# Performance work log

Hardware: AMD Instinct MI355X
Metric: run time of the kernel (lower is better)

Reference implementation:

```python
import jax, jax.numpy as jnp
import numpy as np

N = 100000   # nodes per ntype
E = 1600000  # edges per etype (avg degree 16)
D = 128      # in_channels == hid_channels
LN_EPS = 1e-5


def setup_inputs() -> dict:
    key = jax.random.key(0)
    k = jax.random.split(key, 16)
    scale = 1.0 / np.sqrt(D)
    inp = {
        "x_A": jax.random.normal(k[0], (N, D), jnp.float32),
        "x_B": jax.random.normal(k[1], (N, D), jnp.float32),
        # per-etype GraphConv weights, etype order: [aa, ab, ba, bb]
        "W0": jax.random.normal(k[2], (4, D, D), jnp.float32) * scale,
        "b0": jnp.zeros((4, D), jnp.float32),
        "W1": jax.random.normal(k[3], (4, D, D), jnp.float32) * scale,
        "b1": jnp.zeros((4, D), jnp.float32),
        # LayerNorm params: [layer, ntype(A=0,B=1), D]
        "ln_gamma": jnp.ones((2, 2, D), jnp.float32),
        "ln_beta": jnp.zeros((2, 2, D), jnp.float32),
        "src_aa": jax.random.randint(k[4], (E,), 0, N, jnp.int32),
        "dst_aa": jax.random.randint(k[5], (E,), 0, N, jnp.int32),
        "src_ab": jax.random.randint(k[6], (E,), 0, N, jnp.int32),
        "dst_ab": jax.random.randint(k[7], (E,), 0, N, jnp.int32),
        "src_ba": jax.random.randint(k[8], (E,), 0, N, jnp.int32),
        "dst_ba": jax.random.randint(k[9], (E,), 0, N, jnp.int32),
        "src_bb": jax.random.randint(k[10], (E,), 0, N, jnp.int32),
        "dst_bb": jax.random.randint(k[11], (E,), 0, N, jnp.int32),
    }
    return inp


def _layer_norm(x, g, b):
    m = jnp.mean(x, axis=-1, keepdims=True)
    v = jnp.var(x, axis=-1, keepdims=True)
    return (x - m) * jax.lax.rsqrt(v + LN_EPS) * g + b


def _graph_conv(x, W, b, src, dst, n_dst, act):
    # dgl GraphConv norm='both': D_dst^{-1/2} A D_src^{-1/2} X W + b
    deg_out = jnp.clip(jax.ops.segment_sum(jnp.ones_like(src, x.dtype), src, num_segments=x.shape[0]), 1.0)
    deg_in = jnp.clip(jax.ops.segment_sum(jnp.ones_like(dst, x.dtype), dst, num_segments=n_dst), 1.0)
    h = (x * jax.lax.rsqrt(deg_out)[:, None]) @ W            # transform first (in==out)
    agg = jax.ops.segment_sum(h[src], dst, num_segments=n_dst)
    out = agg * jax.lax.rsqrt(deg_in)[:, None] + b
    return jax.nn.relu(out) if act else out


def reference(x_A, x_B, W0, b0, W1, b1, ln_gamma, ln_beta,
              src_aa, dst_aa, src_ab, dst_ab, src_ba, dst_ba, src_bb, dst_bb):
    hA, hB = x_A, x_B
    for l, (W, bias) in enumerate([(W0, b0), (W1, b1)]):
        act = (l == 0)  # relu inside each GraphConv for all but the last layer
        # HeteroGraphConv aggregate='sum': sum per-relation (activated) outputs per dst ntype
        nA = _graph_conv(hA, W[0], bias[0], src_aa, dst_aa, N, act) + \
             _graph_conv(hB, W[2], bias[2], src_ba, dst_ba, N, act)
        nB = _graph_conv(hA, W[1], bias[1], src_ab, dst_ab, N, act) + \
             _graph_conv(hB, W[3], bias[3], src_bb, dst_bb, N, act)
        hA = _layer_norm(nA, ln_gamma[l, 0], ln_beta[l, 0])
        hB = _layer_norm(nB, ln_gamma[l, 1], ln_beta[l, 1])
        # dropout p=0.0 (eval) -> identity
    return jnp.stack([hA, hB])  # [ntype, N, D]
```

## Files before the change

kernel.cpp:

```cpp
#include <hip/hip_runtime.h>
#include <hip/hip_bf16.h>

#define D 128
typedef unsigned int uint;
typedef unsigned short ushort;
typedef unsigned char uchar;
typedef short short8 __attribute__((ext_vector_type(8)));
typedef float f32x4 __attribute__((ext_vector_type(4)));

#define BKT_SHIFT 8
#define NBMAX 512
#define PART_EPT 16
#define SCAT_CAP 8192

__device__ __forceinline__ ushort f2bf(float f) {
    uint u = __float_as_uint(f);
    return (ushort)((u + 0x7fffu + ((u >> 16) & 1u)) >> 16);
}
__device__ __forceinline__ float bf2f(uint s) { return __uint_as_float(s << 16); }

__global__ __launch_bounds__(256) void bhist4_k(
    const int* __restrict__ s0, const int* __restrict__ d0,
    const int* __restrict__ s1, const int* __restrict__ d1,
    const int* __restrict__ s2, const int* __restrict__ d2,
    const int* __restrict__ s3, const int* __restrict__ d3,
    int* __restrict__ bcs, int* __restrict__ bcd, int N, int E) {
    const int e = blockIdx.y;
    const int* sp = e == 0 ? s0 : e == 1 ? s1 : e == 2 ? s2 : s3;
    const int* dp = e == 0 ? d0 : e == 1 ? d1 : e == 2 ? d2 : d3;
    const int NB = (N + 255) >> BKT_SHIFT;
    __shared__ int hs[NBMAX], hd[NBMAX];
    for (int j = threadIdx.x; j < NBMAX; j += 256) { hs[j] = 0; hd[j] = 0; }
    __syncthreads();
    const int base = blockIdx.x * 8192;
#pragma unroll
    for (int k = 0; k < 8; ++k) {
        int idx = base + (k * 256 + threadIdx.x) * 4;
        if (idx + 4 <= E) {
            int4 s = *(const int4*)(sp + idx);
            int4 d = *(const int4*)(dp + idx);
            atomicAdd(&hs[s.x >> BKT_SHIFT], 1); atomicAdd(&hs[s.y >> BKT_SHIFT], 1);
            atomicAdd(&hs[s.z >> BKT_SHIFT], 1); atomicAdd(&hs[s.w >> BKT_SHIFT], 1);
            atomicAdd(&hd[d.x >> BKT_SHIFT], 1); atomicAdd(&hd[d.y >> BKT_SHIFT], 1);
            atomicAdd(&hd[d.z >> BKT_SHIFT], 1); atomicAdd(&hd[d.w >> BKT_SHIFT], 1);
        } else {
            for (int i = idx; i < E && i < idx + 4; ++i) {
                atomicAdd(&hs[sp[i] >> BKT_SHIFT], 1);
                atomicAdd(&hd[dp[i] >> BKT_SHIFT], 1);
            }
        }
    }
    __syncthreads();
    for (int j = threadIdx.x; j < NB; j += 256) {
        if (hs[j]) atomicAdd(&bcs[e * NBMAX + j], hs[j]);
        if (hd[j]) atomicAdd(&bcd[e * NBMAX + j], hd[j]);
    }
}

__global__ __launch_bounds__(512) void bscan_k(
    const int* __restrict__ bcs, const int* __restrict__ bcd,
    int* __restrict__ sbase, int* __restrict__ scur,
    int* __restrict__ dbase, int* __restrict__ dcur, int N) {
    const int e = blockIdx.y;
    const int side = blockIdx.x;
    const int NB = (N + 255) >> BKT_SHIFT;
    const int* in = (side ? bcd : bcs) + e * NBMAX;
    int* b0 = (side ? dbase : sbase) + e * NBMAX;
    int* c0 = (side ? dcur : scur) + e * NBMAX;
    const int tid = threadIdx.x, lane = tid & 63, wid = tid >> 6;
    int v = (tid < NB) ? in[tid] : 0;
    int x = v;
#pragma unroll
    for (int off = 1; off < 64; off <<= 1) {
        int t = __shfl_up(x, off);
        if (lane >= off) x += t;
    }
    __shared__ int ws[8];
    if (lane == 63) ws[wid] = x;
    __syncthreads();
    if (tid == 0) {
        int run = 0;
#pragma unroll
        for (int w = 0; w < 8; ++w) { int t = ws[w]; ws[w] = run; run += t; }
    }
    __syncthreads();
    int excl = ws[wid] + x - v;
    if (tid < NB) { b0[tid] = excl; c0[tid] = excl; }
}

__global__ __launch_bounds__(256) void part4_k(
    const int* __restrict__ s0, const int* __restrict__ d0,
    const int* __restrict__ s1, const int* __restrict__ d1,
    const int* __restrict__ s2, const int* __restrict__ d2,
    const int* __restrict__ s3, const int* __restrict__ d3,
    int* __restrict__ scur, int* __restrict__ dcur,
    uint* __restrict__ pd, uchar* __restrict__ ps, int N, int E) {
    const int e = blockIdx.y;
    const int* sp = e == 0 ? s0 : e == 1 ? s1 : e == 2 ? s2 : s3;
    const int* dp = e == 0 ? d0 : e == 1 ? d1 : e == 2 ? d2 : d3;
    const int NB = (N + 255) >> BKT_SHIFT;
    uint* ptd = pd + (size_t)e * E;
    uchar* pts = ps + (size_t)e * E;
    __shared__ int hd[NBMAX], hs[NBMAX];
    for (int j = threadIdx.x; j < NBMAX; j += 256) { hd[j] = 0; hs[j] = 0; }
    __syncthreads();
    int myd[PART_EPT], mys[PART_EPT], rkd[PART_EPT], rks[PART_EPT];
    const int base = blockIdx.x * (256 * PART_EPT);
#pragma unroll
    for (int k = 0; k < PART_EPT; ++k) {
        int idx = base + k * 256 + threadIdx.x;
        if (idx < E) {
            int d = dp[idx], s = sp[idx];
            myd[k] = d; mys[k] = s;
            rkd[k] = atomicAdd(&hd[d >> BKT_SHIFT], 1);
            rks[k] = atomicAdd(&hs[s >> BKT_SHIFT], 1);
        } else {
            myd[k] = -1;
        }
    }
    __syncthreads();
    for (int j = threadIdx.x; j < NB; j += 256) {
        int c = hd[j];
        if (c) hd[j] = atomicAdd(&dcur[e * NBMAX + j], c);
        c = hs[j];
        if (c) hs[j] = atomicAdd(&scur[e * NBMAX + j], c);
    }
    __syncthreads();
#pragma unroll
    for (int k = 0; k < PART_EPT; ++k) {
        if (myd[k] >= 0) {
            int d = myd[k], s = mys[k];
            ptd[(size_t)((uint)hd[d >> BKT_SHIFT] + (uint)rkd[k])] =
                ((uint)(d & 255) << 24) | (uint)s;
            pts[(size_t)((uint)hs[s >> BKT_SHIFT] + (uint)rks[k])] = (uchar)(s & 255);
        }
    }
}

__global__ __launch_bounds__(256) void scat4_k(
    const uint* __restrict__ pd, const int* __restrict__ dbase,
    const int* __restrict__ bcd, int* __restrict__ start_g,
    int* __restrict__ cnt_g, float* __restrict__ rs_in,
    int* __restrict__ csr, int N, int E) {
    const int e = blockIdx.y;
    const int b = blockIdx.x;
    const int node0 = b << BKT_SHIFT;
    const int nodes = min(256, N - node0);
    const uint* pt = pd + (size_t)e * E;
    int* out = csr + (size_t)e * E;
    const int csr_base = dbase[e * NBMAX + b];
    const int span = bcd[e * NBMAX + b];
    __shared__ int cnt[256];
    __shared__ int cur[256];
    __shared__ int woff[4];
    __shared__ int lcsr[SCAT_CAP];
    const int tid = threadIdx.x, lane = tid & 63, wid = tid >> 6;
    cnt[tid] = 0;
    __syncthreads();
    for (int i = tid; i < span; i += 256) atomicAdd(&cnt[pt[csr_base + i] >> 24], 1);
    __syncthreads();
    int c = cnt[tid];
    int x = c;
#pragma unroll
    for (int off = 1; off < 64; off <<= 1) {
        int t = __shfl_up(x, off);
        if (lane >= off) x += t;
    }
    if (lane == 63) woff[wid] = x;
    __syncthreads();
    if (tid == 0) {
        int run = 0;
#pragma unroll
        for (int w = 0; w < 4; ++w) { int t = woff[w]; woff[w] = run; run += t; }
    }
    __syncthreads();
    int loc = woff[wid] + x - c;
    cur[tid] = loc;
    if (tid < nodes) {
        int n = node0 + tid;
        start_g[(size_t)e * N + n] = csr_base + loc;
        cnt_g[(size_t)e * N + n] = c;
        rs_in[(size_t)e * N + n] = rsqrtf((float)max(c, 1));
    }
    __syncthreads();
    for (int i = tid; i < span; i += 256) {
        uint pk = pt[csr_base + i];
        int pos = atomicAdd(&cur[pk >> 24], 1);
        int s = (int)(pk & 0xFFFFFFu);
        if (pos < SCAT_CAP) lcsr[pos] = s;
        else out[csr_base + pos] = s;
    }
    __syncthreads();
    const int lim = span < SCAT_CAP ? span : SCAT_CAP;
    for (int i = tid; i < lim; i += 256) out[csr_base + i] = lcsr[i];
}

__global__ __launch_bounds__(256) void shist_k(
    const uchar* __restrict__ ps, const int* __restrict__ sbase,
    const int* __restrict__ bcs, float* __restrict__ rs_out, int N, int E) {
    const int e = blockIdx.y;
    const int b = blockIdx.x;
    const int node0 = b << BKT_SHIFT;
    const int nodes = min(256, N - node0);
    const uchar* pt = ps + (size_t)e * E;
    const int base = sbase[e * NBMAX + b];
    const int span = bcs[e * NBMAX + b];
    __shared__ int c[256];
    c[threadIdx.x] = 0;
    __syncthreads();
    for (int i = threadIdx.x; i < span; i += 256) atomicAdd(&c[pt[base + i]], 1);
    __syncthreads();
    if (threadIdx.x < nodes)
        rs_out[(size_t)e * N + node0 + threadIdx.x] = rsqrtf((float)max(c[threadIdx.x], 1));
}

__global__ __launch_bounds__(256) void wswz_k(const float* __restrict__ W0,
                                              const float* __restrict__ W1,
                                              ushort* __restrict__ WF) {
    int t = blockIdx.x * 256 + threadIdx.x;
    int lane = t & 63, kf = (t >> 6) & 3, ct = (t >> 8) & 7, e = (t >> 11) & 3, l = (t >> 13) & 1;
    const float* Ws = (l ? W1 : W0) + (size_t)e * D * D;
    int m = lane & 15, q = lane >> 4;
    const float* src = Ws + (size_t)(kf * 32 + q * 8) * D + ct * 16 + m;
    ushort v[8];
#pragma unroll
    for (int j = 0; j < 8; ++j) v[j] = f2bf(src[(size_t)j * D]);
    uint4 pk;
    pk.x = (uint)v[0] | ((uint)v[1] << 16);
    pk.y = (uint)v[2] | ((uint)v[3] << 16);
    pk.z = (uint)v[4] | ((uint)v[5] << 16);
    pk.w = (uint)v[6] | ((uint)v[7] << 16);
    *(uint4*)(WF + ((size_t)(l * 4 + e) * 2048 + (ct * 4 + kf) * 64 + lane) * 8) = pk;
}

__global__ __launch_bounds__(256) void gemm_pair_k(
    const float* __restrict__ XA, const float* __restrict__ XB,
    const ushort* __restrict__ WF,
    const float* __restrict__ rs,
    ushort* __restrict__ yb,
    int n) {
    const int p = blockIdx.y;
    const float* X = p ? XB : XA;
    const int e0 = 2 * p, e1 = 2 * p + 1;
    const short8* F0 = (const short8*)(WF + (size_t)e0 * 16384);
    const short8* F1 = (const short8*)(WF + (size_t)e1 * 16384);
    const float* rs0 = rs + (size_t)e0 * n;
    const float* rs1 = rs + (size_t)e1 * n;
    ushort* Y0 = yb + (size_t)e0 * n * D;
    ushort* Y1 = yb + (size_t)e1 * n * D;
    const int lane = threadIdx.x & 63;
    const int m = lane & 15, q = lane >> 4;
    const int wave = blockIdx.x * 4 + (threadIdx.x >> 6);
    const int nw = gridDim.x * 4;
    const int nstrips = (n + 15) >> 4;
    for (int sidx = wave; sidx < nstrips; sidx += nw) {
        const int r = sidx * 16 + m;
        const int rc = r < n ? r : n - 1;
        const float* xp = X + (size_t)rc * D + q * 8;
        short8 xf[4];
#pragma unroll
        for (int kf = 0; kf < 4; ++kf) {
            float4 u0 = *(const float4*)(xp + kf * 32);
            float4 u1 = *(const float4*)(xp + kf * 32 + 4);
            short8 v;
            v[0] = (short)f2bf(u0.x); v[1] = (short)f2bf(u0.y);
            v[2] = (short)f2bf(u0.z); v[3] = (short)f2bf(u0.w);
            v[4] = (short)f2bf(u1.x); v[5] = (short)f2bf(u1.y);
            v[6] = (short)f2bf(u1.z); v[7] = (short)f2bf(u1.w);
            xf[kf] = v;
        }
        f32x4 a0[8], a1[8];
#pragma unroll
        for (int ct = 0; ct < 8; ++ct) {
            a0[ct] = (f32x4){0.f, 0.f, 0.f, 0.f};
            a1[ct] = (f32x4){0.f, 0.f, 0.f, 0.f};
        }
#pragma unroll
        for (int ct = 0; ct < 8; ++ct)
#pragma unroll
            for (int kf = 0; kf < 4; ++kf) {
                a0[ct] = __builtin_amdgcn_mfma_f32_16x16x32_bf16(
                    F0[(ct * 4 + kf) * 64 + lane], xf[kf], a0[ct], 0, 0, 0);
                a1[ct] = __builtin_amdgcn_mfma_f32_16x16x32_bf16(
                    F1[(ct * 4 + kf) * 64 + lane], xf[kf], a1[ct], 0, 0, 0);
            }
        if (r < n) {
            float s0v = rs0[r], s1v = rs1[r];
            ushort* y0r = Y0 + (size_t)r * D + q * 4;
            ushort* y1r = Y1 + (size_t)r * D + q * 4;
#pragma unroll
            for (int ct = 0; ct < 8; ++ct) {
                uint2 w;
                w.x = (uint)f2bf(a0[ct][0] * s0v) | ((uint)f2bf(a0[ct][1] * s0v) << 16);
                w.y = (uint)f2bf(a0[ct][2] * s0v) | ((uint)f2bf(a0[ct][3] * s0v) << 16);
                *(uint2*)(y0r + ct * 16) = w;
                uint2 z;
                z.x = (uint)f2bf(a1[ct][0] * s1v) | ((uint)f2bf(a1[ct][1] * s1v) << 16);
                z.y = (uint)f2bf(a1[ct][2] * s1v) | ((uint)f2bf(a1[ct][3] * s1v) << 16);
                *(uint2*)(y1r + ct * 16) = z;
            }
        }
    }
}

__global__ __launch_bounds__(256) void agg_ln2_k(
    const ushort* __restrict__ yb, const int* __restrict__ csr,
    const int* __restrict__ start, const int* __restrict__ cnt,
    const float* __restrict__ rs_in, const float* __restrict__ bias,
    const float* __restrict__ lng, const float* __restrict__ lnb,
    float* __restrict__ outA, float* __restrict__ outB,
    int N, int E, int act, int layer) {
    const int dt = blockIdx.y;
    const int eA = dt, eB = dt + 2;
    const int lane = threadIdx.x & 63;
    const int row = blockIdx.x * 4 + (threadIdx.x >> 6);
    if (row >= N) return;
    const uint* YuA = (const uint*)(yb + (size_t)eA * N * D);
    const uint* YuB = (const uint*)(yb + (size_t)eB * N * D);
    const int* cAp = csr + (size_t)eA * E;
    const int* cBp = csr + (size_t)eB * E;
    int iA = start[(size_t)eA * N + row], enA = iA + cnt[(size_t)eA * N + row];
    int iB = start[(size_t)eB * N + row], enB = iB + cnt[(size_t)eB * N + row];
    float a0 = 0.f, a1 = 0.f, c0 = 0.f, c1 = 0.f;
    while (iA + 4 <= enA && iB + 4 <= enB) {
        int sa0 = cAp[iA], sa1 = cAp[iA + 1], sa2 = cAp[iA + 2], sa3 = cAp[iA + 3];
        int sb0 = cBp[iB], sb1 = cBp[iB + 1], sb2 = cBp[iB + 2], sb3 = cBp[iB + 3];
        uint pa0 = YuA[(size_t)sa0 * 64 + lane], pa1 = YuA[(size_t)sa1 * 64 + lane];
        uint pa2 = YuA[(size_t)sa2 * 64 + lane], pa3 = YuA[(size_t)sa3 * 64 + lane];
        uint pb0 = YuB[(size_t)sb0 * 64 + lane], pb1 = YuB[(size_t)sb1 * 64 + lane];
        uint pb2 = YuB[(size_t)sb2 * 64 + lane], pb3 = YuB[(size_t)sb3 * 64 + lane];
        a0 += bf2f(pa0 & 0xffffu) + bf2f(pa1 & 0xffffu) + bf2f(pa2 & 0xffffu) + bf2f(pa3 & 0xffffu);
        a1 += bf2f(pa0 >> 16) + bf2f(pa1 >> 16) + bf2f(pa2 >> 16) + bf2f(pa3 >> 16);
        c0 += bf2f(pb0 & 0xffffu) + bf2f(pb1 & 0xffffu) + bf2f(pb2 & 0xffffu) + bf2f(pb3 & 0xffffu);
        c1 += bf2f(pb0 >> 16) + bf2f(pb1 >> 16) + bf2f(pb2 >> 16) + bf2f(pb3 >> 16);
        iA += 4; iB += 4;
    }
    for (; iA + 4 <= enA; iA += 4) {
        int s0 = cAp[iA], s1 = cAp[iA + 1], s2 = cAp[iA + 2], s3 = cAp[iA + 3];
        uint p0 = YuA[(size_t)s0 * 64 + lane], p1 = YuA[(size_t)s1 * 64 + lane];
        uint p2 = YuA[(size_t)s2 * 64 + lane], p3 = YuA[(size_t)s3 * 64 + lane];
        a0 += bf2f(p0 & 0xffffu) + bf2f(p1 & 0xffffu) + bf2f(p2 & 0xffffu) + bf2f(p3 & 0xffffu);
        a1 += bf2f(p0 >> 16) + bf2f(p1 >> 16) + bf2f(p2 >> 16) + bf2f(p3 >> 16);
    }
    for (; iB + 4 <= enB; iB += 4) {
        int s0 = cBp[iB], s1 = cBp[iB + 1], s2 = cBp[iB + 2], s3 = cBp[iB + 3];
        uint p0 = YuB[(size_t)s0 * 64 + lane], p1 = YuB[(size_t)s1 * 64 + lane];
        uint p2 = YuB[(size_t)s2 * 64 + lane], p3 = YuB[(size_t)s3 * 64 + lane];
        c0 += bf2f(p0 & 0xffffu) + bf2f(p1 & 0xffffu) + bf2f(p2 & 0xffffu) + bf2f(p3 & 0xffffu);
        c1 += bf2f(p0 >> 16) + bf2f(p1 >> 16) + bf2f(p2 >> 16) + bf2f(p3 >> 16);
    }
    for (; iA < enA; ++iA) {
        uint p = YuA[(size_t)cAp[iA] * 64 + lane];
        a0 += bf2f(p & 0xffffu); a1 += bf2f(p >> 16);
    }
    for (; iB < enB; ++iB) {
        uint p = YuB[(size_t)cBp[iB] * 64 + lane];
        c0 += bf2f(p & 0xffffu); c1 += bf2f(p >> 16);
    }
    float riA = rs_in[(size_t)eA * N + row], riB = rs_in[(size_t)eB * N + row];
    float2 bA = *(const float2*)(bias + eA * D + lane * 2);
    float2 bB = *(const float2*)(bias + eB * D + lane * 2);
    float v0 = fmaf(a0, riA, bA.x), v1 = fmaf(a1, riA, bA.y);
    float w0 = fmaf(c0, riB, bB.x), w1 = fmaf(c1, riB, bB.y);
    if (act) {
        v0 = fmaxf(v0, 0.f); v1 = fmaxf(v1, 0.f);
        w0 = fmaxf(w0, 0.f); w1 = fmaxf(w1, 0.f);
    }
    v0 += w0; v1 += w1;
    float s = v0 + v1, qq = v0 * v0 + v1 * v1;
#pragma unroll
    for (int off = 1; off < 64; off <<= 1) {
        s += __shfl_xor(s, off);
        qq += __shfl_xor(qq, off);
    }
    float mean = s * (1.f / 128.f);
    float var = qq * (1.f / 128.f) - mean * mean;
    float inv = rsqrtf(var + 1e-5f);
    const int gi = (layer * 2 + dt) * D + lane * 2;
    float2 g = *(const float2*)(lng + gi);
    float2 be = *(const float2*)(lnb + gi);
    float2 o;
    o.x = fmaf((v0 - mean) * inv, g.x, be.x);
    o.y = fmaf((v1 - mean) * inv, g.y, be.y);
    float* OUT = dt ? outB : outA;
    *(float2*)(OUT + (size_t)row * D + lane * 2) = o;
}

extern "C" void kernel_launch(void* const* d_in, const int* in_sizes, int n_in,
                              void* d_out, int out_size, void* d_ws, size_t ws_size,
                              hipStream_t stream) {
    const int N = in_sizes[0] / D;
    const int E = in_sizes[8];
    const float* xA = (const float*)d_in[0];
    const float* xB = (const float*)d_in[1];
    const float* W0 = (const float*)d_in[2];
    const float* b0 = (const float*)d_in[3];
    const float* W1 = (const float*)d_in[4];
    const float* b1 = (const float*)d_in[5];
    const float* lng = (const float*)d_in[6];
    const float* lnb = (const float*)d_in[7];
    const int* s_aa = (const int*)d_in[8];
    const int* d_aa = (const int*)d_in[9];
    const int* s_ab = (const int*)d_in[10];
    const int* d_ab = (const int*)d_in[11];
    const int* s_ba = (const int*)d_in[12];
    const int* d_ba = (const int*)d_in[13];
    const int* s_bb = (const int*)d_in[14];
    const int* d_bb = (const int*)d_in[15];

    const size_t nd = (size_t)N * D;
    char* p = (char*)d_ws;
    ushort* y = (ushort*)p;
    p += 4 * nd * sizeof(ushort);
    ushort* WF = (ushort*)p;
    p += 2 * 4 * 2048 * 8 * sizeof(ushort);
    int* bcnt_s = (int*)p;
    int* bcnt_d = bcnt_s + 4 * NBMAX;
    int* sbase = bcnt_d + 4 * NBMAX;
    int* scur = sbase + 4 * NBMAX;
    int* dbase = scur + 4 * NBMAX;
    int* dcur = dbase + 4 * NBMAX;
    int* start_g = dcur + 4 * NBMAX;
    int* cnt_g = start_g + 4 * (size_t)N;
    p = (char*)(cnt_g + 4 * (size_t)N);
    float* rs_out = (float*)p;
    float* rs_in = rs_out + 4 * (size_t)N;
    p = (char*)(rs_in + 4 * (size_t)N);
    int* csr = (int*)p;
    uint* part_d = (uint*)y;
    uchar* part_s = (uchar*)(part_d + 4 * (size_t)E);

    float* hA = (float*)d_out;
    float* hB = hA + nd;

    hipMemsetAsync(bcnt_s, 0, 2 * 4 * NBMAX * sizeof(int), stream);

    const int TB = 256;
    const int NBn = (N + 255) >> BKT_SHIFT;

    dim3 bhg((E + 8191) / 8192, 4);
    bhist4_k<<<bhg, TB, 0, stream>>>(s_aa, d_aa, s_ab, d_ab, s_ba, d_ba, s_bb, d_bb,
                                     bcnt_s, bcnt_d, N, E);
    dim3 bsg(2, 4);
    bscan_k<<<bsg, 512, 0, stream>>>(bcnt_s, bcnt_d, sbase, scur, dbase, dcur, N);
    dim3 pg4((E + 256 * PART_EPT - 1) / (256 * PART_EPT), 4);
    part4_k<<<pg4, TB, 0, stream>>>(s_aa, d_aa, s_ab, d_ab, s_ba, d_ba, s_bb, d_bb,
                                    scur, dcur, part_d, part_s, N, E);
    dim3 scg4(NBn, 4);
    scat4_k<<<scg4, TB, 0, stream>>>(part_d, dbase, bcnt_d, start_g, cnt_g, rs_in,
                                     csr, N, E);
    shist_k<<<scg4, TB, 0, stream>>>(part_s, sbase, bcnt_s, rs_out, N, E);
    wswz_k<<<64, TB, 0, stream>>>(W0, W1, WF);

    dim3 gg(384, 2);
    dim3 ag((N + 3) / 4, 2);
    const size_t WFL = 4 * 2048 * 8;

    gemm_pair_k<<<gg, TB, 0, stream>>>(xA, xB, WF, rs_out, y, N);
    agg_ln2_k<<<ag, TB, 0, stream>>>(y, csr, start_g, cnt_g, rs_in, b0,
                                     lng, lnb, hA, hB, N, E, 1, 0);
    gemm_pair_k<<<gg, TB, 0, stream>>>(hA, hB, WF + WFL, rs_out, y, N);
    agg_ln2_k<<<ag, TB, 0, stream>>>(y, csr, start_g, cnt_g, rs_in, b1,
                                     lng, lnb, hA, hB, N, E, 0, 1);
}
```

Before: 954.0 us.

## Stage partition writes through shared memory and gather 4 neighbors per wave with uint4 loads

The partition kernel now does a block-local exclusive scan over bucket counts and stages records in LDS sorted by bucket. It then writes them to global memory in order, so the scattered stores coalesce into contiguous runs. The aggregation kernel splits each wave into four 16-lane groups, each fetching a whole 256-byte bf16 row with uint4 loads, then reduces across groups with shuffles. This cuts the number of load instructions per edge, but adds LDS usage (about 40KB per partition block), extra barriers, and a cross-group reduction in which three quarters of the lanes do redundant LayerNorm work.

```diff
diff --git a/kernel.cpp b/kernel.cpp
--- a/kernel.cpp
+++ b/kernel.cpp
@@ -11,6 +11,7 @@
 #define BKT_SHIFT 8
 #define NBMAX 512
 #define PART_EPT 16
+#define EPB 4096
 #define SCAT_CAP 8192
 
 __device__ __forceinline__ ushort f2bf(float f) {
@@ -88,6 +89,32 @@
     if (tid < NB) { b0[tid] = excl; c0[tid] = excl; }
 }
 
+__device__ __forceinline__ void scan_reserve(int* h, int* gcur, int* Lb, int* Gb,
+                                             int* ws) {
+    const int t = threadIdx.x, lane = t & 63, wid = t >> 6;
+    int c0 = h[2 * t], c1 = h[2 * t + 1];
+    int tsum = c0 + c1;
+    int x = tsum;
+#pragma unroll
+    for (int off = 1; off < 64; off <<= 1) {
+        int u = __shfl_up(x, off);
+        if (lane >= off) x += u;
+    }
+    if (lane == 63) ws[wid] = x;
+    __syncthreads();
+    if (t == 0) {
+        int run = 0;
+#pragma unroll
+        for (int w = 0; w < 4; ++w) { int u = ws[w]; ws[w] = run; run += u; }
+    }
+    __syncthreads();
+    int excl = ws[wid] + x - tsum;
+    Lb[2 * t] = excl;
+    Lb[2 * t + 1] = excl + c0;
+    Gb[2 * t] = c0 ? atomicAdd(&gcur[2 * t], c0) : 0;
+    Gb[2 * t + 1] = c1 ? atomicAdd(&gcur[2 * t + 1], c1) : 0;
+}
+
 __global__ __launch_bounds__(256) void part4_k(
     const int* __restrict__ s0, const int* __restrict__ d0,
     const int* __restrict__ s1, const int* __restrict__ d1,
@@ -98,14 +125,18 @@
     const int e = blockIdx.y;
     const int* sp = e == 0 ? s0 : e == 1 ? s1 : e == 2 ? s2 : s3;
     const int* dp = e == 0 ? d0 : e == 1 ? d1 : e == 2 ? d2 : d3;
-    const int NB = (N + 255) >> BKT_SHIFT;
     uint* ptd = pd + (size_t)e * E;
     uchar* pts = ps + (size_t)e * E;
     __shared__ int hd[NBMAX], hs[NBMAX];
+    __shared__ int Lb[NBMAX], Gb[NBMAX];
+    __shared__ uint rec[EPB];
+    __shared__ int dst[EPB];
+    __shared__ int ws[4];
     for (int j = threadIdx.x; j < NBMAX; j += 256) { hd[j] = 0; hs[j] = 0; }
     __syncthreads();
     int myd[PART_EPT], mys[PART_EPT], rkd[PART_EPT], rks[PART_EPT];
-    const int base = blockIdx.x * (256 * PART_EPT);
+    const int base = blockIdx.x * EPB;
+    const int nE = min(EPB, E - base);
 #pragma unroll
     for (int k = 0; k < PART_EPT; ++k) {
         int idx = base + k * 256 + threadIdx.x;
@@ -119,22 +150,33 @@
         }
     }
     __syncthreads();
-    for (int j = threadIdx.x; j < NB; j += 256) {
-        int c = hd[j];
-        if (c) hd[j] = atomicAdd(&dcur[e * NBMAX + j], c);
-        c = hs[j];
-        if (c) hs[j] = atomicAdd(&scur[e * NBMAX + j], c);
-    }
+    scan_reserve(hd, dcur + e * NBMAX, Lb, Gb, ws);
     __syncthreads();
 #pragma unroll
     for (int k = 0; k < PART_EPT; ++k) {
         if (myd[k] >= 0) {
-            int d = myd[k], s = mys[k];
-            ptd[(size_t)((uint)hd[d >> BKT_SHIFT] + (uint)rkd[k])] =
-                ((uint)(d & 255) << 24) | (uint)s;
-            pts[(size_t)((uint)hs[s >> BKT_SHIFT] + (uint)rks[k])] = (uchar)(s & 255);
-        }
-    }
+            int b = myd[k] >> BKT_SHIFT;
+            int q = Lb[b] + rkd[k];
+            rec[q] = ((uint)(myd[k] & 255) << 24) | (uint)mys[k];
+            dst[q] = Gb[b] + rkd[k];
+        }
+    }
+    __syncthreads();
+    for (int i = threadIdx.x; i < nE; i += 256) ptd[dst[i]] = rec[i];
+    __syncthreads();
+    scan_reserve(hs, scur + e * NBMAX, Lb, Gb, ws);
+    __syncthreads();
+#pragma unroll
+    for (int k = 0; k < PART_EPT; ++k) {
+        if (myd[k] >= 0) {
+            int b = mys[k] >> BKT_SHIFT;
+            int q = Lb[b] + rks[k];
+            rec[q] = (uint)(mys[k] & 255);
+            dst[q] = Gb[b] + rks[k];
+        }
+    }
+    __syncthreads();
+    for (int i = threadIdx.x; i < nE; i += 256) pts[dst[i]] = (uchar)rec[i];
 }
 
 __global__ __launch_bounds__(256) void scat4_k(
@@ -303,7 +345,13 @@
     }
 }
 
-__global__ __launch_bounds__(256) void agg_ln2_k(
+#define ACC8(acc, u)                                                     \
+    acc[0] += bf2f(u.x & 0xffffu); acc[1] += bf2f(u.x >> 16);            \
+    acc[2] += bf2f(u.y & 0xffffu); acc[3] += bf2f(u.y >> 16);            \
+    acc[4] += bf2f(u.z & 0xffffu); acc[5] += bf2f(u.z >> 16);            \
+    acc[6] += bf2f(u.w & 0xffffu); acc[7] += bf2f(u.w >> 16);
+
+__global__ __launch_bounds__(256) void agg_ln4_k(
     const ushort* __restrict__ yb, const int* __restrict__ csr,
     const int* __restrict__ start, const int* __restrict__ cnt,
     const float* __restrict__ rs_in, const float* __restrict__ bias,
@@ -313,77 +361,95 @@
     const int dt = blockIdx.y;
     const int eA = dt, eB = dt + 2;
     const int lane = threadIdx.x & 63;
+    const int grp = lane >> 4, m = lane & 15;
     const int row = blockIdx.x * 4 + (threadIdx.x >> 6);
     if (row >= N) return;
-    const uint* YuA = (const uint*)(yb + (size_t)eA * N * D);
-    const uint* YuB = (const uint*)(yb + (size_t)eB * N * D);
+    const uint4* YA = (const uint4*)(yb + (size_t)eA * N * D);
+    const uint4* YB = (const uint4*)(yb + (size_t)eB * N * D);
     const int* cAp = csr + (size_t)eA * E;
     const int* cBp = csr + (size_t)eB * E;
     int iA = start[(size_t)eA * N + row], enA = iA + cnt[(size_t)eA * N + row];
     int iB = start[(size_t)eB * N + row], enB = iB + cnt[(size_t)eB * N + row];
-    float a0 = 0.f, a1 = 0.f, c0 = 0.f, c1 = 0.f;
-    while (iA + 4 <= enA && iB + 4 <= enB) {
-        int sa0 = cAp[iA], sa1 = cAp[iA + 1], sa2 = cAp[iA + 2], sa3 = cAp[iA + 3];
-        int sb0 = cBp[iB], sb1 = cBp[iB + 1], sb2 = cBp[iB + 2], sb3 = cBp[iB + 3];
-        uint pa0 = YuA[(size_t)sa0 * 64 + lane], pa1 = YuA[(size_t)sa1 * 64 + lane];
-        uint pa2 = YuA[(size_t)sa2 * 64 + lane], pa3 = YuA[(size_t)sa3 * 64 + lane];
-        uint pb0 = YuB[(size_t)sb0 * 64 + lane], pb1 = YuB[(size_t)sb1 * 64 + lane];
-        uint pb2 = YuB[(size_t)sb2 * 64 + lane], pb3 = YuB[(size_t)sb3 * 64 + lane];
-        a0 += bf2f(pa0 & 0xffffu) + bf2f(pa1 & 0xffffu) + bf2f(pa2 & 0xffffu) + bf2f(pa3 & 0xffffu);
-        a1 += bf2f(pa0 >> 16) + bf2f(pa1 >> 16) + bf2f(pa2 >> 16) + bf2f(pa3 >> 16);
-        c0 += bf2f(pb0 & 0xffffu) + bf2f(pb1 & 0xffffu) + bf2f(pb2 & 0xffffu) + bf2f(pb3 & 0xffffu);
-        c1 += bf2f(pb0 >> 16) + bf2f(pb1 >> 16) + bf2f(pb2 >> 16) + bf2f(pb3 >> 16);
-        iA += 4; iB += 4;
-    }
+    float aA[8] = {0.f, 0.f, 0.f, 0.f, 0.f, 0.f, 0.f, 0.f};
+    float aB[8] = {0.f, 0.f, 0.f, 0.f, 0.f, 0.f, 0.f, 0.f};
     for (; iA + 4 <= enA; iA += 4) {
-        int s0 = cAp[iA], s1 = cAp[iA + 1], s2 = cAp[iA + 2], s3 = cAp[iA + 3];
-        uint p0 = YuA[(size_t)s0 * 64 + lane], p1 = YuA[(size_t)s1 * 64 + lane];
-        uint p2 = YuA[(size_t)s2 * 64 + lane], p3 = YuA[(size_t)s3 * 64 + lane];
-        a0 += bf2f(p0 & 0xffffu) + bf2f(p1 & 0xffffu) + bf2f(p2 & 0xffffu) + bf2f(p3 & 0xffffu);
-        a1 += bf2f(p0 >> 16) + bf2f(p1 >> 16) + bf2f(p2 >> 16) + bf2f(p3 >> 16);
+        int s = cAp[iA + grp];
+        uint4 u = YA[(size_t)s * 16 + m];
+        ACC8(aA, u)
+    }
+    {
+        int remA = enA - iA;
+        if (grp < remA) {
+            int s = cAp[iA + grp];
+            uint4 u = YA[(size_t)s * 16 + m];
+            ACC8(aA, u)
+        }
     }
     for (; iB + 4 <= enB; iB += 4) {
-        int s0 = cBp[iB], s1 = cBp[iB + 1], s2 = cBp[iB + 2], s3 = cBp[iB + 3];
-        uint p0 = YuB[(size_t)s0 * 64 + lane], p1 = YuB[(size_t)s1 * 64 + lane];
-        uint p2 = YuB[(size_t)s2 * 64 + lane], p3 = YuB[(size_t)s3 * 64 + lane];
-        c0 += bf2f(p0 & 0xffffu) + bf2f(p1 & 0xffffu) + bf2f(p2 & 0xffffu) + bf2f(p3 & 0xffffu);
-        c1 += bf2f(p0 >> 16) + bf2f(p1 >> 16) + bf2f(p2 >> 16) + bf2f(p3 >> 16);
-    }
-    for (; iA < enA; ++iA) {
-        uint p = YuA[(size_t)cAp[iA] * 64 + lane];
-        a0 += bf2f(p & 0xffffu); a1 += bf2f(p >> 16);
-    }
-    for (; iB < enB; ++iB) {
-        uint p = YuB[(size_t)cBp[iB] * 64 + lane];
-        c0 += bf2f(p & 0xffffu); c1 += bf2f(p >> 16);
+        int s = cBp[iB + grp];
+        uint4 u = YB[(size_t)s * 16 + m];
+        ACC8(aB, u)
+    }
+    {
+        int remB = enB - iB;
+        if (grp < remB) {
+            int s = cBp[iB + grp];
+            uint4 u = YB[(size_t)s * 16 + m];
+            ACC8(aB, u)
+        }
+    }
+#pragma unroll
+    for (int j = 0; j < 8; ++j) {
+        aA[j] += __shfl_xor(aA[j], 16); aA[j] += __shfl_xor(aA[j], 32);
+        aB[j] += __shfl_xor(aB[j], 16); aB[j] += __shfl_xor(aB[j], 32);
     }
     float riA = rs_in[(size_t)eA * N + row], riB = rs_in[(size_t)eB * N + row];
-    float2 bA = *(const float2*)(bias + eA * D + lane * 2);
-    float2 bB = *(const float2*)(bias + eB * D + lane * 2);
-    float v0 = fmaf(a0, riA, bA.x), v1 = fmaf(a1, riA, bA.y);
-    float w0 = fmaf(c0, riB, bB.x), w1 = fmaf(c1, riB, bB.y);
-    if (act) {
-        v0 = fmaxf(v0, 0.f); v1 = fmaxf(v1, 0.f);
-        w0 = fmaxf(w0, 0.f); w1 = fmaxf(w1, 0.f);
-    }
-    v0 += w0; v1 += w1;
-    float s = v0 + v1, qq = v0 * v0 + v1 * v1;
-#pragma unroll
-    for (int off = 1; off < 64; off <<= 1) {
+    float4 bA0 = *(const float4*)(bias + eA * D + m * 8);
+    float4 bA1 = *(const float4*)(bias + eA * D + m * 8 + 4);
+    float4 bB0 = *(const float4*)(bias + eB * D + m * 8);
+    float4 bB1 = *(const float4*)(bias + eB * D + m * 8 + 4);
+    float bAv[8] = {bA0.x, bA0.y, bA0.z, bA0.w, bA1.x, bA1.y, bA1.z, bA1.w};
+    float bBv[8] = {bB0.x, bB0.y, bB0.z, bB0.w, bB1.x, bB1.y, bB1.z, bB1.w};
+    float v[8];
+#pragma unroll
+    for (int j = 0; j < 8; ++j) {
+        float x = fmaf(aA[j], riA, bAv[j]);
+        float w = fmaf(aB[j], riB, bBv[j]);
+        if (act) { x = fmaxf(x, 0.f); w = fmaxf(w, 0.f); }
+        v[j] = x + w;
+    }
+    float s = 0.f, qq = 0.f;
+#pragma unroll
+    for (int j = 0; j < 8; ++j) { s += v[j]; qq += v[j] * v[j]; }
+#pragma unroll
+    for (int off = 1; off < 16; off <<= 1) {
         s += __shfl_xor(s, off);
         qq += __shfl_xor(qq, off);
     }
     float mean = s * (1.f / 128.f);
     float var = qq * (1.f / 128.f) - mean * mean;
     float inv = rsqrtf(var + 1e-5f);
-    const int gi = (layer * 2 + dt) * D + lane * 2;
-    float2 g = *(const float2*)(lng + gi);
-    float2 be = *(const float2*)(lnb + gi);
-    float2 o;
-    o.x = fmaf((v0 - mean) * inv, g.x, be.x);
-    o.y = fmaf((v1 - mean) * inv, g.y, be.y);
-    float* OUT = dt ? outB : outA;
-    *(float2*)(OUT + (size_t)row * D + lane * 2) = o;
+    const int gi = (layer * 2 + dt) * D + m * 8;
+    float4 g0 = *(const float4*)(lng + gi);
+    float4 g1 = *(const float4*)(lng + gi + 4);
+    float4 be0 = *(const float4*)(lnb + gi);
+    float4 be1 = *(const float4*)(lnb + gi + 4);
+    float gv[8] = {g0.x, g0.y, g0.z, g0.w, g1.x, g1.y, g1.z, g1.w};
+    float bev[8] = {be0.x, be0.y, be0.z, be0.w, be1.x, be1.y, be1.z, be1.w};
+    if (grp == 0) {
+        float4 o0, o1;
+        o0.x = fmaf((v[0] - mean) * inv, gv[0], bev[0]);
+        o0.y = fmaf((v[1] - mean) * inv, gv[1], bev[1]);
+        o0.z = fmaf((v[2] - mean) * inv, gv[2], bev[2]);
+        o0.w = fmaf((v[3] - mean) * inv, gv[3], bev[3]);
+        o1.x = fmaf((v[4] - mean) * inv, gv[4], bev[4]);
+        o1.y = fmaf((v[5] - mean) * inv, gv[5], bev[5]);
+        o1.z = fmaf((v[6] - mean) * inv, gv[6], bev[6]);
+        o1.w = fmaf((v[7] - mean) * inv, gv[7], bev[7]);
+        float* OUT = dt ? outB : outA;
+        *(float4*)(OUT + (size_t)row * D + m * 8) = o0;
+        *(float4*)(OUT + (size_t)row * D + m * 8 + 4) = o1;
+    }
 }
 
 extern "C" void kernel_launch(void* const* d_in, const int* in_sizes, int n_in,
@@ -443,7 +509,7 @@
                                      bcnt_s, bcnt_d, N, E);
     dim3 bsg(2, 4);
     bscan_k<<<bsg, 512, 0, stream>>>(bcnt_s, bcnt_d, sbase, scur, dbase, dcur, N);
-    dim3 pg4((E + 256 * PART_EPT - 1) / (256 * PART_EPT), 4);
+    dim3 pg4((E + EPB - 1) / EPB, 4);
     part4_k<<<pg4, TB, 0, stream>>>(s_aa, d_aa, s_ab, d_ab, s_ba, d_ba, s_bb, d_bb,
                                     scur, dcur, part_d, part_s, N, E);
     dim3 scg4(NBn, 4);
@@ -457,9 +523,9 @@
     const size_t WFL = 4 * 2048 * 8;
 
     gemm_pair_k<<<gg, TB, 0, stream>>>(xA, xB, WF, rs_out, y, N);
-    agg_ln2_k<<<ag, TB, 0, stream>>>(y, csr, start_g, cnt_g, rs_in, b0,
+    agg_ln4_k<<<ag, TB, 0, stream>>>(y, csr, start_g, cnt_g, rs_in, b0,
                                      lng, lnb, hA, hB, N, E, 1, 0);
     gemm_pair_k<<<gg, TB, 0, stream>>>(hA, hB, WF + WFL, rs_out, y, N);
-    agg_ln2_k<<<ag, TB, 0, stream>>>(y, csr, start_g, cnt_g, rs_in, b1,
+    agg_ln4_k<<<ag, TB, 0, stream>>>(y, csr, start_g, cnt_g, rs_in, b1,
                                      lng, lnb, hA, hB, N, E, 0, 1);
 }
```

After: 977.2 us. +2.4%, slower.

## Stage partition writes in LDS, fuse source histogram, keep layer-0 output in bf16

Applied to the files above, without the earlier changes.

The partition kernel now does a block-local scan per bucket and sorts its records in shared memory. Each bucket's records then go to global memory as one contiguous run, replacing scattered per-element writes. The source-degree histogram kernel is merged into the CSR scatter kernel, which removes one launch and one pass. The layer-0 LayerNorm output is written as a bf16 intermediate that the layer-1 GEMM reads directly, halving that round trip's traffic. The cost is much more LDS in the partition kernel (about 40KB), which lowers occupancy.

```diff
diff --git a/kernel.cpp b/kernel.cpp
--- a/kernel.cpp
+++ b/kernel.cpp
@@ -11,6 +11,7 @@
 #define BKT_SHIFT 8
 #define NBMAX 512
 #define PART_EPT 16
+#define EPB 4096
 #define SCAT_CAP 8192
 
 __device__ __forceinline__ ushort f2bf(float f) {
@@ -88,6 +89,32 @@
     if (tid < NB) { b0[tid] = excl; c0[tid] = excl; }
 }
 
+__device__ __forceinline__ void scan_reserve(int* h, int* gcur, int* Lb, int* Gb,
+                                             int* ws) {
+    const int t = threadIdx.x, lane = t & 63, wid = t >> 6;
+    int c0 = h[2 * t], c1 = h[2 * t + 1];
+    int tsum = c0 + c1;
+    int x = tsum;
+#pragma unroll
+    for (int off = 1; off < 64; off <<= 1) {
+        int u = __shfl_up(x, off);
+        if (lane >= off) x += u;
+    }
+    if (lane == 63) ws[wid] = x;
+    __syncthreads();
+    if (t == 0) {
+        int run = 0;
+#pragma unroll
+        for (int w = 0; w < 4; ++w) { int u = ws[w]; ws[w] = run; run += u; }
+    }
+    __syncthreads();
+    int excl = ws[wid] + x - tsum;
+    Lb[2 * t] = excl;
+    Lb[2 * t + 1] = excl + c0;
+    Gb[2 * t] = c0 ? atomicAdd(&gcur[2 * t], c0) : 0;
+    Gb[2 * t + 1] = c1 ? atomicAdd(&gcur[2 * t + 1], c1) : 0;
+}
+
 __global__ __launch_bounds__(256) void part4_k(
     const int* __restrict__ s0, const int* __restrict__ d0,
     const int* __restrict__ s1, const int* __restrict__ d1,
@@ -98,14 +125,18 @@
     const int e = blockIdx.y;
     const int* sp = e == 0 ? s0 : e == 1 ? s1 : e == 2 ? s2 : s3;
     const int* dp = e == 0 ? d0 : e == 1 ? d1 : e == 2 ? d2 : d3;
-    const int NB = (N + 255) >> BKT_SHIFT;
     uint* ptd = pd + (size_t)e * E;
     uchar* pts = ps + (size_t)e * E;
     __shared__ int hd[NBMAX], hs[NBMAX];
+    __shared__ int Lb[NBMAX], Gb[NBMAX];
+    __shared__ uint rec[EPB];
+    __shared__ int dst[EPB];
+    __shared__ int ws[4];
     for (int j = threadIdx.x; j < NBMAX; j += 256) { hd[j] = 0; hs[j] = 0; }
     __syncthreads();
     int myd[PART_EPT], mys[PART_EPT], rkd[PART_EPT], rks[PART_EPT];
-    const int base = blockIdx.x * (256 * PART_EPT);
+    const int base = blockIdx.x * EPB;
+    const int nE = min(EPB, E - base);
 #pragma unroll
     for (int k = 0; k < PART_EPT; ++k) {
         int idx = base + k * 256 + threadIdx.x;
@@ -119,28 +150,42 @@
         }
     }
     __syncthreads();
-    for (int j = threadIdx.x; j < NB; j += 256) {
-        int c = hd[j];
-        if (c) hd[j] = atomicAdd(&dcur[e * NBMAX + j], c);
-        c = hs[j];
-        if (c) hs[j] = atomicAdd(&scur[e * NBMAX + j], c);
-    }
+    scan_reserve(hd, dcur + e * NBMAX, Lb, Gb, ws);
     __syncthreads();
 #pragma unroll
     for (int k = 0; k < PART_EPT; ++k) {
         if (myd[k] >= 0) {
-            int d = myd[k], s = mys[k];
-            ptd[(size_t)((uint)hd[d >> BKT_SHIFT] + (uint)rkd[k])] =
-                ((uint)(d & 255) << 24) | (uint)s;
-            pts[(size_t)((uint)hs[s >> BKT_SHIFT] + (uint)rks[k])] = (uchar)(s & 255);
-        }
-    }
-}
-
-__global__ __launch_bounds__(256) void scat4_k(
+            int b = myd[k] >> BKT_SHIFT;
+            int q = Lb[b] + rkd[k];
+            rec[q] = ((uint)(myd[k] & 255) << 24) | (uint)mys[k];
+            dst[q] = Gb[b] + rkd[k];
+        }
+    }
+    __syncthreads();
+    for (int i = threadIdx.x; i < nE; i += 256) ptd[dst[i]] = rec[i];
+    __syncthreads();
+    scan_reserve(hs, scur + e * NBMAX, Lb, Gb, ws);
+    __syncthreads();
+#pragma unroll
+    for (int k = 0; k < PART_EPT; ++k) {
+        if (myd[k] >= 0) {
+            int b = mys[k] >> BKT_SHIFT;
+            int q = Lb[b] + rks[k];
+            rec[q] = (uint)(mys[k] & 255);
+            dst[q] = Gb[b] + rks[k];
+        }
+    }
+    __syncthreads();
+    for (int i = threadIdx.x; i < nE; i += 256) pts[dst[i]] = (uchar)rec[i];
+}
+
+__global__ __launch_bounds__(256) void scatsh_k(
     const uint* __restrict__ pd, const int* __restrict__ dbase,
-    const int* __restrict__ bcd, int* __restrict__ start_g,
-    int* __restrict__ cnt_g, float* __restrict__ rs_in,
+    const int* __restrict__ bcd,
+    const uchar* __restrict__ ps, const int* __restrict__ sbase,
+    const int* __restrict__ bcs,
+    int* __restrict__ start_g, int* __restrict__ cnt_g,
+    float* __restrict__ rs_in, float* __restrict__ rs_out,
     int* __restrict__ csr, int N, int E) {
     const int e = blockIdx.y;
     const int b = blockIdx.x;
@@ -152,13 +197,23 @@
     const int span = bcd[e * NBMAX + b];
     __shared__ int cnt[256];
     __shared__ int cur[256];
+    __shared__ int cs[256];
     __shared__ int woff[4];
     __shared__ int lcsr[SCAT_CAP];
     const int tid = threadIdx.x, lane = tid & 63, wid = tid >> 6;
     cnt[tid] = 0;
+    cs[tid] = 0;
     __syncthreads();
     for (int i = tid; i < span; i += 256) atomicAdd(&cnt[pt[csr_base + i] >> 24], 1);
-    __syncthreads();
+    {
+        const uchar* pts = ps + (size_t)e * E;
+        const int sb = sbase[e * NBMAX + b];
+        const int sspan = bcs[e * NBMAX + b];
+        for (int i = tid; i < sspan; i += 256) atomicAdd(&cs[pts[sb + i]], 1);
+    }
+    __syncthreads();
+    if (tid < nodes)
+        rs_out[(size_t)e * N + node0 + tid] = rsqrtf((float)max(cs[tid], 1));
     int c = cnt[tid];
     int x = c;
 #pragma unroll
@@ -193,25 +248,6 @@
     __syncthreads();
     const int lim = span < SCAT_CAP ? span : SCAT_CAP;
     for (int i = tid; i < lim; i += 256) out[csr_base + i] = lcsr[i];
-}
-
-__global__ __launch_bounds__(256) void shist_k(
-    const uchar* __restrict__ ps, const int* __restrict__ sbase,
-    const int* __restrict__ bcs, float* __restrict__ rs_out, int N, int E) {
-    const int e = blockIdx.y;
-    const int b = blockIdx.x;
-    const int node0 = b << BKT_SHIFT;
-    const int nodes = min(256, N - node0);
-    const uchar* pt = ps + (size_t)e * E;
-    const int base = sbase[e * NBMAX + b];
-    const int span = bcs[e * NBMAX + b];
-    __shared__ int c[256];
-    c[threadIdx.x] = 0;
-    __syncthreads();
-    for (int i = threadIdx.x; i < span; i += 256) atomicAdd(&c[pt[base + i]], 1);
-    __syncthreads();
-    if (threadIdx.x < nodes)
-        rs_out[(size_t)e * N + node0 + threadIdx.x] = rsqrtf((float)max(c[threadIdx.x], 1));
 }
 
 __global__ __launch_bounds__(256) void wswz_k(const float* __restrict__ W0,
@@ -234,13 +270,15 @@
 }
 
 __global__ __launch_bounds__(256) void gemm_pair_k(
-    const float* __restrict__ XA, const float* __restrict__ XB,
+    const float* __restrict__ XAf, const float* __restrict__ XBf,
+    const ushort* __restrict__ Xb, int bf16in,
     const ushort* __restrict__ WF,
     const float* __restrict__ rs,
     ushort* __restrict__ yb,
     int n) {
     const int p = blockIdx.y;
-    const float* X = p ? XB : XA;
+    const float* Xf = p ? XBf : XAf;
+    const ushort* Xh = Xb + (size_t)p * n * D;
     const int e0 = 2 * p, e1 = 2 * p + 1;
     const short8* F0 = (const short8*)(WF + (size_t)e0 * 16384);
     const short8* F1 = (const short8*)(WF + (size_t)e1 * 16384);
@@ -256,18 +294,24 @@
     for (int sidx = wave; sidx < nstrips; sidx += nw) {
         const int r = sidx * 16 + m;
         const int rc = r < n ? r : n - 1;
-        const float* xp = X + (size_t)rc * D + q * 8;
         short8 xf[4];
-#pragma unroll
-        for (int kf = 0; kf < 4; ++kf) {
-            float4 u0 = *(const float4*)(xp + kf * 32);
-            float4 u1 = *(const float4*)(xp + kf * 32 + 4);
-            short8 v;
-            v[0] = (short)f2bf(u0.x); v[1] = (short)f2bf(u0.y);
-            v[2] = (short)f2bf(u0.z); v[3] = (short)f2bf(u0.w);
-            v[4] = (short)f2bf(u1.x); v[5] = (short)f2bf(u1.y);
-            v[6] = (short)f2bf(u1.z); v[7] = (short)f2bf(u1.w);
-            xf[kf] = v;
+        if (bf16in) {
+            const ushort* xp = Xh + (size_t)rc * D + q * 8;
+#pragma unroll
+            for (int kf = 0; kf < 4; ++kf) xf[kf] = *(const short8*)(xp + kf * 32);
+        } else {
+            const float* xp = Xf + (size_t)rc * D + q * 8;
+#pragma unroll
+            for (int kf = 0; kf < 4; ++kf) {
+                float4 u0 = *(const float4*)(xp + kf * 32);
+                float4 u1 = *(const float4*)(xp + kf * 32 + 4);
+                short8 v;
+                v[0] = (short)f2bf(u0.x); v[1] = (short)f2bf(u0.y);
+                v[2] = (short)f2bf(u0.z); v[3] = (short)f2bf(u0.w);
+                v[4] = (short)f2bf(u1.x); v[5] = (short)f2bf(u1.y);
+                v[6] = (short)f2bf(u1.z); v[7] = (short)f2bf(u1.w);
+                xf[kf] = v;
+            }
         }
         f32x4 a0[8], a1[8];
 #pragma unroll
@@ -308,8 +352,8 @@
     const int* __restrict__ start, const int* __restrict__ cnt,
     const float* __restrict__ rs_in, const float* __restrict__ bias,
     const float* __restrict__ lng, const float* __restrict__ lnb,
-    float* __restrict__ outA, float* __restrict__ outB,
-    int N, int E, int act, int layer) {
+    ushort* __restrict__ hb, float* __restrict__ outA, float* __restrict__ outB,
+    int N, int E, int act, int layer, int outbf) {
     const int dt = blockIdx.y;
     const int eA = dt, eB = dt + 2;
     const int lane = threadIdx.x & 63;
@@ -379,11 +423,16 @@
     const int gi = (layer * 2 + dt) * D + lane * 2;
     float2 g = *(const float2*)(lng + gi);
     float2 be = *(const float2*)(lnb + gi);
-    float2 o;
-    o.x = fmaf((v0 - mean) * inv, g.x, be.x);
-    o.y = fmaf((v1 - mean) * inv, g.y, be.y);
-    float* OUT = dt ? outB : outA;
-    *(float2*)(OUT + (size_t)row * D + lane * 2) = o;
+    float o0 = fmaf((v0 - mean) * inv, g.x, be.x);
+    float o1 = fmaf((v1 - mean) * inv, g.y, be.y);
+    if (outbf) {
+        uint* H = (uint*)(hb + (size_t)dt * N * D);
+        H[(size_t)row * 64 + lane] = (uint)f2bf(o0) | ((uint)f2bf(o1) << 16);
+    } else {
+        float* OUT = dt ? outB : outA;
+        float2 o; o.x = o0; o.y = o1;
+        *(float2*)(OUT + (size_t)row * D + lane * 2) = o;
+    }
 }
 
 extern "C" void kernel_launch(void* const* d_in, const int* in_sizes, int n_in,
@@ -412,6 +461,8 @@
     char* p = (char*)d_ws;
     ushort* y = (ushort*)p;
     p += 4 * nd * sizeof(ushort);
+    ushort* hb = (ushort*)p;
+    p += 2 * nd * sizeof(ushort);
     ushort* WF = (ushort*)p;
     p += 2 * 4 * 2048 * 8 * sizeof(ushort);
     int* bcnt_s = (int*)p;
@@ -443,23 +494,22 @@
                                      bcnt_s, bcnt_d, N, E);
     dim3 bsg(2, 4);
     bscan_k<<<bsg, 512, 0, stream>>>(bcnt_s, bcnt_d, sbase, scur, dbase, dcur, N);
-    dim3 pg4((E + 256 * PART_EPT - 1) / (256 * PART_EPT), 4);
+    dim3 pg4((E + EPB - 1) / EPB, 4);
     part4_k<<<pg4, TB, 0, stream>>>(s_aa, d_aa, s_ab, d_ab, s_ba, d_ba, s_bb, d_bb,
                                     scur, dcur, part_d, part_s, N, E);
     dim3 scg4(NBn, 4);
-    scat4_k<<<scg4, TB, 0, stream>>>(part_d, dbase, bcnt_d, start_g, cnt_g, rs_in,
-                                     csr, N, E);
-    shist_k<<<scg4, TB, 0, stream>>>(part_s, sbase, bcnt_s, rs_out, N, E);
+    scatsh_k<<<scg4, TB, 0, stream>>>(part_d, dbase, bcnt_d, part_s, sbase, bcnt_s,
+                                      start_g, cnt_g, rs_in, rs_out, csr, N, E);
     wswz_k<<<64, TB, 0, stream>>>(W0, W1, WF);
 
     dim3 gg(384, 2);
     dim3 ag((N + 3) / 4, 2);
     const size_t WFL = 4 * 2048 * 8;
 
-    gemm_pair_k<<<gg, TB, 0, stream>>>(xA, xB, WF, rs_out, y, N);
+    gemm_pair_k<<<gg, TB, 0, stream>>>(xA, xB, hb, 0, WF, rs_out, y, N);
     agg_ln2_k<<<ag, TB, 0, stream>>>(y, csr, start_g, cnt_g, rs_in, b0,
-                                     lng, lnb, hA, hB, N, E, 1, 0);
-    gemm_pair_k<<<gg, TB, 0, stream>>>(hA, hB, WF + WFL, rs_out, y, N);
+                                     lng, lnb, hb, hA, hB, N, E, 1, 0, 1);
+    gemm_pair_k<<<gg, TB, 0, stream>>>(xA, xB, hb, 1, WF + WFL, rs_out, y, N);
     agg_ln2_k<<<ag, TB, 0, stream>>>(y, csr, start_g, cnt_g, rs_in, b1,
-                                     lng, lnb, hA, hB, N, E, 0, 1);
-}
+                                     lng, lnb, hb, hA, hB, N, E, 0, 1, 0);
+}
```

New measurement: 891.2 us (median of 2 runs). 1.07x faster.
